# Performance work log

Hardware: AMD Instinct MI355X
Metric: run time of the kernel (lower is better)

Reference implementation:

```python
import jax, jax.numpy as jnp
import numpy as np

B, C, H, Wd = 4, 2048, 64, 64
HID = 256


def setup_inputs() -> dict:
    key = jax.random.key(0)
    k1, k2, k3, k4 = jax.random.split(key, 4)
    return {
        "query_features": jax.random.normal(k1, (B, C, H, Wd), dtype=jnp.float32),
        "prompt_features": jax.random.normal(k2, (B, C, H, Wd), dtype=jnp.float32),
        "W": jax.random.normal(k3, (HID, C), dtype=jnp.float32) * (1.0 / np.sqrt(C)),
        "b": jax.random.normal(k4, (HID,), dtype=jnp.float32) * 0.02,
    }


def reference(query_features, prompt_features, W, b):
    # 1x1 conv == channel projection
    Q = jnp.einsum('bchw,oc->bohw', query_features, W) + b[None, :, None, None]
    K = jnp.einsum('bchw,oc->bohw', prompt_features, W) + b[None, :, None, None]
    Bq, Cf, Hq, Wq = prompt_features.shape
    V = prompt_features.reshape(Bq, Cf, Hq * Wq)              # b c p
    # full pairwise score tensor: bijkl -> b i j (k l)
    attn = jnp.einsum('bcij,bckl->bijkl', Q, K).reshape(Bq, Hq, Wq, Hq * Wq)
    attn = jax.nn.softmax(attn, axis=3)
    aligned = jnp.einsum('bijp,bcp->bcij', attn, V)           # b c h w
    return aligned
```

## Files before the change

### kernel.cpp

```cpp
#include <hip/hip_runtime.h>
#include <math.h>


#define BATCH 4
#define CH    2048
#define PP    4096
#define DD    256

typedef __bf16    bf16x8 __attribute__((ext_vector_type(8)));
typedef _Float16  f16x8  __attribute__((ext_vector_type(8)));
typedef _Float16  f16x4  __attribute__((ext_vector_type(4)));
typedef float     f32x4  __attribute__((ext_vector_type(4)));

__device__ __forceinline__ unsigned short f2bf(float f) {
  unsigned int u = __float_as_uint(f);
  unsigned int r = u + 0x7fffu + ((u >> 16) & 1u);
  return (unsigned short)(r >> 16);
}

#define GLL(src, dst) \
  __builtin_amdgcn_global_load_lds( \
      (const __attribute__((address_space(1))) unsigned int*)(uintptr_t)(src), \
      (__attribute__((address_space(3))) unsigned int*)(uintptr_t)(dst), 16, 0, 0)

__global__ __launch_bounds__(256) void prep_w(
    const float* __restrict__ W, _Float16* __restrict__ Wf) {
  int i = blockIdx.x * 256 + threadIdx.x;
  float4 v = ((const float4*)W)[i];
  f16x4 h = {(_Float16)v.x, (_Float16)v.y, (_Float16)v.z, (_Float16)v.w};
  ((f16x4*)Wf)[i] = h;
}

__global__ __launch_bounds__(256) void projX(
    const float* __restrict__ Xq, const float* __restrict__ Xp,
    const _Float16* __restrict__ Wf, const float* __restrict__ bias,
    unsigned short* __restrict__ Qh, unsigned short* __restrict__ Ql,
    unsigned short* __restrict__ Kh, unsigned short* __restrict__ Kl,
    unsigned short* __restrict__ Vb8, int zbase, int single) {
  const int z = zbase + blockIdx.z;
  const int b = z >> 1;
  const int ob = single ? 0 : b;
  const float* __restrict__ X =
      ((z & 1) ? Xp : Xq) + (size_t)b * CH * PP;
  unsigned short* __restrict__ Yh =
      ((z & 1) ? Kh : Qh) + (size_t)ob * PP * DD;
  unsigned short* __restrict__ Yl =
      ((z & 1) ? Kl : Ql) + (size_t)ob * PP * DD;
  unsigned short* __restrict__ Vb = Vb8 + (size_t)ob * CH * PP;
  const int emitV = (z & 1);

  const int pBase = blockIdx.x * 64;
  const int tid  = threadIdx.x;
  const int wave = tid >> 6;
  const int lane = tid & 63;
  const int row16 = lane & 15, quad = lane >> 4;

  __shared__ __align__(16) char LdsP[32768 + 16384];
  char*  Ws  = LdsP;
  float* LsX = (float*)(LdsP + 32768);

  const int wRowIn  = lane >> 3;
  const int wChunk  = (((lane & 7) ^ (lane >> 3)) << 4);
  const int xRowIn  = lane >> 4;
  const int xColB   = (lane & 15) * 16;

  f32x4 acc[4][4];
#pragma unroll
  for (int i = 0; i < 4; ++i)
#pragma unroll
    for (int j = 0; j < 4; ++j) acc[i][j] = (f32x4){0.f, 0.f, 0.f, 0.f};

#pragma unroll 1
  for (int c0 = 0; c0 < CH; c0 += 64) {
#pragma unroll
    for (int q = 0; q < 8; ++q) {
      const int g = wave * 8 + q;
      const char* src = (const char*)Wf +
          (size_t)(g * 8 + wRowIn) * (CH * 2) + c0 * 2 + wChunk;
      GLL(src, Ws + g * 1024);
    }
#pragma unroll
    for (int q = 0; q < 4; ++q) {
      const int g = wave * 4 + q;
      const char* src = (const char*)X +
          ((size_t)(c0 + g * 4 + xRowIn) * PP + pBase) * 4 + xColB;
      GLL(src, (char*)LsX + g * 1024);
    }
    __syncthreads();

#pragma unroll
    for (int s = 0; s < 2; ++s) {
      f16x8 af[4], bf[4];
#pragma unroll
      for (int i = 0; i < 4; ++i) {
        f16x8 a;
#pragma unroll
        for (int e = 0; e < 8; ++e)
          a[e] = (_Float16)LsX[(s * 32 + quad * 8 + e) * 64 + i * 16 + row16];
        af[i] = a;
      }
#pragma unroll
      for (int j = 0; j < 4; ++j) {
        const int brow = wave * 64 + j * 16 + row16;
        bf[j] = *(const f16x8*)(Ws + brow * 128 +
                                (((s * 4 + quad) ^ (row16 & 7)) << 4));
      }
#pragma unroll
      for (int i = 0; i < 4; ++i)
#pragma unroll
        for (int j = 0; j < 4; ++j)
          acc[i][j] = __builtin_amdgcn_mfma_f32_16x16x32_f16(
              af[i], bf[j], acc[i][j], 0, 0, 0);
    }

    if (emitV) {
      const int cl = tid >> 2, ps = (tid & 3) * 16;
      const float* xr = &LsX[cl * 64 + ps];
      unsigned short tmp[16];
#pragma unroll
      for (int u = 0; u < 16; ++u) tmp[u] = f2bf(xr[u]);
      char* dst = (char*)Vb + ((size_t)(c0 + cl) * PP + pBase + ps) * 2;
      *(uint4*)dst        = *(const uint4*)tmp;
      *(uint4*)(dst + 16) = *(const uint4*)(tmp + 8);
    }
    __syncthreads();
  }

#pragma unroll
  for (int i = 0; i < 4; ++i)
#pragma unroll
    for (int j = 0; j < 4; ++j) {
      const int ocol = wave * 64 + j * 16 + row16;
      const float bv = bias[ocol];
#pragma unroll
      for (int r = 0; r < 4; ++r) {
        const int prow = pBase + i * 16 + quad * 4 + r;
        float y = acc[i][j][r] + bv;
        unsigned short h = f2bf(y);
        float hf = __uint_as_float((unsigned int)h << 16);
        unsigned short l = f2bf(y - hf);
        Yh[(size_t)prow * DD + ocol] = h;
        Yl[(size_t)prow * DD + ocol] = l;
      }
    }
}

__global__ __launch_bounds__(256) void softmax8(float* __restrict__ S_) {
  float* __restrict__ Sb = S_ + (size_t)blockIdx.y * PP * PP;
  unsigned short* __restrict__ Ab = (unsigned short*)Sb;
  const size_t p = blockIdx.x;
  float* row = Sb + p * PP;
  const int tid = threadIdx.x;
  float4 v[4];
#pragma unroll
  for (int i = 0; i < 4; ++i)
    v[i] = *(const float4*)&row[(i * 256 + tid) * 4];
  float m = -1e30f;
#pragma unroll
  for (int i = 0; i < 4; ++i)
    m = fmaxf(m, fmaxf(fmaxf(v[i].x, v[i].y), fmaxf(v[i].z, v[i].w)));
#pragma unroll
  for (int off = 32; off > 0; off >>= 1)
    m = fmaxf(m, __shfl_xor(m, off));
  __shared__ float red[4];
  const int lane = tid & 63, wv = tid >> 6;
  if (lane == 0) red[wv] = m;
  __syncthreads();
  m = fmaxf(fmaxf(red[0], red[1]), fmaxf(red[2], red[3]));
  __syncthreads();
  float s = 0.f;
#pragma unroll
  for (int i = 0; i < 4; ++i) {
    v[i].x = __expf(v[i].x - m);
    v[i].y = __expf(v[i].y - m);
    v[i].z = __expf(v[i].z - m);
    v[i].w = __expf(v[i].w - m);
    s += v[i].x + v[i].y + v[i].z + v[i].w;
  }
#pragma unroll
  for (int off = 32; off > 0; off >>= 1)
    s += __shfl_xor(s, off);
  if (lane == 0) red[wv] = s;
  __syncthreads();
  s = red[0] + red[1] + red[2] + red[3];
  const float inv = 1.f / s;
  unsigned short* orow = Ab + p * 8192;
#pragma unroll
  for (int i = 0; i < 4; ++i) {
    ushort4 o;
    o.x = f2bf(v[i].x * inv); o.y = f2bf(v[i].y * inv);
    o.z = f2bf(v[i].z * inv); o.w = f2bf(v[i].w * inv);
    *(ushort4*)&orow[(i * 256 + tid) * 4] = o;
  }
}


#define AOFF(d, h) ((d) * 32768 + (h) * 16384)
#define BOFF(d, h) (65536 + (d) * 32768 + (h) * 16384)

#define PH_READ_A(d, mh) do {                                                  \
  _Pragma("unroll")                                                            \
  for (int m_ = 0; m_ < 4; ++m_) {                                             \
    const int ro_ = AOFF(d, wm) + ((mh) * 64 + m_ * 16 + row16) * 128;         \
    aR[m_][0] = *(const bf16x8*)(Lds + ro_ + cx0);                             \
    aR[m_][1] = *(const bf16x8*)(Lds + ro_ + cx1);                             \
  } } while (0)

#define PH_READ_B(d, nh, breg) do {                                            \
  _Pragma("unroll")                                                            \
  for (int n_ = 0; n_ < 2; ++n_) {                                             \
    const int ro_ = BOFF(d, wnh) + (wnl * 64 + (nh) * 32 + n_ * 16 + row16) * 128; \
    breg[n_][0] = *(const bf16x8*)(Lds + ro_ + cx0);                           \
    breg[n_][1] = *(const bf16x8*)(Lds + ro_ + cx1);                           \
  } } while (0)

#define PH_MFMA(mh, nh, breg) do {                                             \
  __builtin_amdgcn_s_setprio(1);                                               \
  _Pragma("unroll")                                                            \
  for (int m_ = 0; m_ < 4; ++m_)                                               \
  _Pragma("unroll")                                                            \
  for (int n_ = 0; n_ < 2; ++n_) {                                             \
    f32x4 a_ = acc[(mh) * 4 + m_][(nh) * 2 + n_];                              \
    a_ = __builtin_amdgcn_mfma_f32_16x16x32_bf16(aR[m_][0], breg[n_][0], a_, 0, 0, 0); \
    a_ = __builtin_amdgcn_mfma_f32_16x16x32_bf16(aR[m_][1], breg[n_][1], a_, 0, 0, 0); \
    acc[(mh) * 4 + m_][(nh) * 2 + n_] = a_;                                    \
  }                                                                            \
  __builtin_amdgcn_s_setprio(0); } while (0)

#define PH_MFMA3(mh, nh, breg) do {                                            \
  __builtin_amdgcn_s_setprio(1);                                               \
  _Pragma("unroll")                                                            \
  for (int m_ = 0; m_ < 4; ++m_)                                               \
  _Pragma("unroll")                                                            \
  for (int n_ = 0; n_ < 2; ++n_) {                                             \
    f32x4 a_ = acc[(mh) * 4 + m_][(nh) * 2 + n_];                              \
    a_ = __builtin_amdgcn_mfma_f32_16x16x32_bf16(aR[m_][0], breg[n_][0], a_, 0, 0, 0); \
    a_ = __builtin_amdgcn_mfma_f32_16x16x32_bf16(aR[m_][0], breg[n_][1], a_, 0, 0, 0); \
    a_ = __builtin_amdgcn_mfma_f32_16x16x32_bf16(aR[m_][1], breg[n_][0], a_, 0, 0, 0); \
    acc[(mh) * 4 + m_][(nh) * 2 + n_] = a_;                                    \
  }                                                                            \
  __builtin_amdgcn_s_setprio(0); } while (0)

#define BAR_MID() do {                                                         \
  __builtin_amdgcn_sched_barrier(0);                                           \
  __builtin_amdgcn_s_barrier();                                                \
  asm volatile("s_waitcnt lgkmcnt(0)" ::: "memory");                           \
  __builtin_amdgcn_sched_barrier(0); } while (0)

#define BAR_END() __builtin_amdgcn_s_barrier()

__global__ __launch_bounds__(512, 2) void out8(
    const unsigned short* __restrict__ V_,
    const unsigned short* __restrict__ A_,
    float* __restrict__ O_) {
  const size_t z = blockIdx.z;
  const unsigned short* __restrict__ Vb = V_ + z * (size_t)CH * PP;
  const unsigned short* __restrict__ Ab = A_ + z * (size_t)PP * 8192;
  float* __restrict__ Ob = O_ + z * (size_t)CH * PP;

  const int pBase = blockIdx.x * 256;
  const int cBase = blockIdx.y * 256;
  const int tid = threadIdx.x;
  const int wave = tid >> 6, lane = tid & 63;
  const int wm = wave >> 2;
  const int wn = wave & 3;
  const int wnh = wn >> 1, wnl = wn & 1;
  const int row16 = lane & 15, quad = lane >> 4;

  __shared__ __align__(16) char Lds[131072];

  const int swz = (row16 & 7) << 4;
  const int cx0 = ((quad) << 4) ^ swz;
  const int cx1 = ((4 + quad) << 4) ^ swz;

  const int stRow0 = (wave * 2 + 0) * 8 + (lane >> 3);
  const int stRow1 = (wave * 2 + 1) * 8 + (lane >> 3);
  const int stCol  = (((lane & 7) ^ (lane >> 3)) << 4);
  char* ldsSt0 = Lds + (wave * 2 + 0) * 1024;
  char* ldsSt1 = Lds + (wave * 2 + 1) * 1024;

  const size_t VLDG = (size_t)PP * 2;
  const size_t ALDG = (size_t)8192 * 2;

  auto STG = [&](int ldsOff, const void* gbase, size_t ldgB, int rowBase, int gkB) {
    const char* g0 = (const char*)gbase + (size_t)(rowBase + stRow0) * ldgB + gkB + stCol;
    const char* g1 = (const char*)gbase + (size_t)(rowBase + stRow1) * ldgB + gkB + stCol;
    GLL(g0, ldsSt0 + ldsOff);
    GLL(g1, ldsSt1 + ldsOff);
  };

  f32x4 acc[8][4];
#pragma unroll
  for (int i = 0; i < 8; ++i)
#pragma unroll
    for (int j = 0; j < 4; ++j) acc[i][j] = (f32x4){0.f, 0.f, 0.f, 0.f};

  bf16x8 aR[4][2], bLo[2][2], bHi[2][2];

  STG(BOFF(0, 0), Ab, ALDG, pBase + 0,   0);
  STG(BOFF(0, 1), Ab, ALDG, pBase + 128, 0);
  STG(AOFF(0, 0), Vb, VLDG, cBase + 0,   0);
  STG(AOFF(0, 1), Vb, VLDG, cBase + 128, 0);
  STG(BOFF(1, 0), Ab, ALDG, pBase + 0,   128);
  STG(BOFF(1, 1), Ab, ALDG, pBase + 128, 128);
  asm volatile("s_waitcnt vmcnt(4)" ::: "memory");
  __builtin_amdgcn_s_barrier();

#pragma unroll 1
  for (int i = 0; i < 31; ++i) {
    const int t = 2 * i;
    const int gk1 = (t + 1) * 128, gk2 = (t + 2) * 128, gk3 = (t + 3) * 128;
    PH_READ_A(0, 0); PH_READ_B(0, 0, bLo);
    STG(AOFF(1, 0), Vb, VLDG, cBase + 0, gk1);
    BAR_MID(); PH_MFMA(0, 0, bLo); BAR_END();
    PH_READ_B(0, 1, bHi);
    STG(AOFF(1, 1), Vb, VLDG, cBase + 128, gk1);
    BAR_MID(); PH_MFMA(0, 1, bHi); BAR_END();
    PH_READ_A(0, 1);
    STG(BOFF(0, 0), Ab, ALDG, pBase + 0, gk2);
    BAR_MID(); PH_MFMA(1, 0, bLo); BAR_END();
    STG(BOFF(0, 1), Ab, ALDG, pBase + 128, gk2);
    BAR_MID(); PH_MFMA(1, 1, bHi);
    asm volatile("s_waitcnt vmcnt(4)" ::: "memory");
    BAR_END();
    PH_READ_A(1, 0); PH_READ_B(1, 0, bLo);
    STG(AOFF(0, 0), Vb, VLDG, cBase + 0, gk2);
    BAR_MID(); PH_MFMA(0, 0, bLo); BAR_END();
    PH_READ_B(1, 1, bHi);
    STG(AOFF(0, 1), Vb, VLDG, cBase + 128, gk2);
    BAR_MID(); PH_MFMA(0, 1, bHi); BAR_END();
    PH_READ_A(1, 1);
    STG(BOFF(1, 0), Ab, ALDG, pBase + 0, gk3);
    BAR_MID(); PH_MFMA(1, 0, bLo); BAR_END();
    STG(BOFF(1, 1), Ab, ALDG, pBase + 128, gk3);
    BAR_MID(); PH_MFMA(1, 1, bHi);
    asm volatile("s_waitcnt vmcnt(4)" ::: "memory");
    BAR_END();
  }

  {
    const int gk1 = 63 * 128;
    PH_READ_A(0, 0); PH_READ_B(0, 0, bLo);
    STG(AOFF(1, 0), Vb, VLDG, cBase + 0, gk1);
    BAR_MID(); PH_MFMA(0, 0, bLo); BAR_END();
    PH_READ_B(0, 1, bHi);
    STG(AOFF(1, 1), Vb, VLDG, cBase + 128, gk1);
    BAR_MID(); PH_MFMA(0, 1, bHi); BAR_END();
    PH_READ_A(0, 1);
    BAR_MID(); PH_MFMA(1, 0, bLo); BAR_END();
    BAR_MID(); PH_MFMA(1, 1, bHi);
    asm volatile("s_waitcnt vmcnt(0)" ::: "memory");
    BAR_END();
    PH_READ_A(1, 0); PH_READ_B(1, 0, bLo);
    BAR_MID(); PH_MFMA(0, 0, bLo); BAR_END();
    PH_READ_B(1, 1, bHi);
    BAR_MID(); PH_MFMA(0, 1, bHi); BAR_END();
    PH_READ_A(1, 1);
    BAR_MID(); PH_MFMA(1, 0, bLo); BAR_END();
    BAR_MID(); PH_MFMA(1, 1, bHi);
  }

#pragma unroll
  for (int mi = 0; mi < 8; ++mi)
#pragma unroll
    for (int nj = 0; nj < 4; ++nj) {
      const int col = pBase + wn * 64 + nj * 16 + row16;
      float* orow = Ob + (size_t)(cBase + wm * 128 + mi * 16 + quad * 4) * PP + col;
#pragma unroll
      for (int r = 0; r < 4; ++r)
        orow[(size_t)r * PP] = acc[mi][nj][r];
    }
}

__global__ __launch_bounds__(512, 2) void scr8(
    const unsigned short* __restrict__ Qh_, const unsigned short* __restrict__ Ql_,
    const unsigned short* __restrict__ Kh_, const unsigned short* __restrict__ Kl_,
    float* __restrict__ S_) {
  const size_t z = blockIdx.z;
  const unsigned short* __restrict__ Qh = Qh_ + z * (size_t)PP * DD;
  const unsigned short* __restrict__ Ql = Ql_ + z * (size_t)PP * DD;
  const unsigned short* __restrict__ Kh = Kh_ + z * (size_t)PP * DD;
  const unsigned short* __restrict__ Kl = Kl_ + z * (size_t)PP * DD;
  float* __restrict__ S = S_ + z * (size_t)PP * PP;

  const int kBase = blockIdx.x * 256;
  const int pBase = blockIdx.y * 256;
  const int tid = threadIdx.x;
  const int wave = tid >> 6, lane = tid & 63;
  const int wm = wave >> 2;
  const int wn = wave & 3;
  const int wnh = wn >> 1, wnl = wn & 1;
  const int row16 = lane & 15, quad = lane >> 4;

  __shared__ __align__(16) char Lds[131072];

  const int swz = (row16 & 7) << 4;
  const int cx0 = ((quad) << 4) ^ swz;
  const int cx1 = ((4 + quad) << 4) ^ swz;

  const int stRow0 = (wave * 2 + 0) * 8 + (lane >> 3);
  const int stRow1 = (wave * 2 + 1) * 8 + (lane >> 3);
  const int cc   = (lane & 7) ^ (lane >> 3);
  const int ccB  = (cc & 3) * 16;
  const char* tQ = (const char*)((cc >> 2) ? Ql : Qh);
  const char* tK = (const char*)((cc >> 2) ? Kl : Kh);
  char* ldsSt0 = Lds + (wave * 2 + 0) * 1024;
  char* ldsSt1 = Lds + (wave * 2 + 1) * 1024;

  auto STG = [&](int ldsOff, const char* tbase, int rowBase, int tkB) {
    const char* g0 = tbase + (size_t)(rowBase + stRow0) * 512 + tkB + ccB;
    const char* g1 = tbase + (size_t)(rowBase + stRow1) * 512 + tkB + ccB;
    GLL(g0, ldsSt0 + ldsOff);
    GLL(g1, ldsSt1 + ldsOff);
  };

  f32x4 acc[8][4];
#pragma unroll
  for (int i = 0; i < 8; ++i)
#pragma unroll
    for (int j = 0; j < 4; ++j) acc[i][j] = (f32x4){0.f, 0.f, 0.f, 0.f};

  bf16x8 aR[4][2], bLo[2][2], bHi[2][2];

  STG(BOFF(0, 0), tK, kBase + 0,   0);
  STG(BOFF(0, 1), tK, kBase + 128, 0);
  STG(AOFF(0, 0), tQ, pBase + 0,   0);
  STG(AOFF(0, 1), tQ, pBase + 128, 0);
  STG(BOFF(1, 0), tK, kBase + 0,   64);
  STG(BOFF(1, 1), tK, kBase + 128, 64);
  asm volatile("s_waitcnt vmcnt(4)" ::: "memory");
  __builtin_amdgcn_s_barrier();

#pragma unroll 1
  for (int i = 0; i < 3; ++i) {
    const int t = 2 * i;
    const int gk1 = (t + 1) * 64, gk2 = (t + 2) * 64, gk3 = (t + 3) * 64;
    PH_READ_A(0, 0); PH_READ_B(0, 0, bLo);
    STG(AOFF(1, 0), tQ, pBase + 0, gk1);
    BAR_MID(); PH_MFMA3(0, 0, bLo); BAR_END();
    PH_READ_B(0, 1, bHi);
    STG(AOFF(1, 1), tQ, pBase + 128, gk1);
    BAR_MID(); PH_MFMA3(0, 1, bHi); BAR_END();
    PH_READ_A(0, 1);
    STG(BOFF(0, 0), tK, kBase + 0, gk2);
    BAR_MID(); PH_MFMA3(1, 0, bLo); BAR_END();
    STG(BOFF(0, 1), tK, kBase + 128, gk2);
    BAR_MID(); PH_MFMA3(1, 1, bHi);
    asm volatile("s_waitcnt vmcnt(4)" ::: "memory");
    BAR_END();
    PH_READ_A(1, 0); PH_READ_B(1, 0, bLo);
    STG(AOFF(0, 0), tQ, pBase + 0, gk2);
    BAR_MID(); PH_MFMA3(0, 0, bLo); BAR_END();
    PH_READ_B(1, 1, bHi);
    STG(AOFF(0, 1), tQ, pBase + 128, gk2);
    BAR_MID(); PH_MFMA3(0, 1, bHi); BAR_END();
    PH_READ_A(1, 1);
    STG(BOFF(1, 0), tK, kBase + 0, gk3);
    BAR_MID(); PH_MFMA3(1, 0, bLo); BAR_END();
    STG(BOFF(1, 1), tK, kBase + 128, gk3);
    BAR_MID(); PH_MFMA3(1, 1, bHi);
    asm volatile("s_waitcnt vmcnt(4)" ::: "memory");
    BAR_END();
  }

  {
    const int gk1 = 7 * 64;
    PH_READ_A(0, 0); PH_READ_B(0, 0, bLo);
    STG(AOFF(1, 0), tQ, pBase + 0, gk1);
    BAR_MID(); PH_MFMA3(0, 0, bLo); BAR_END();
    PH_READ_B(0, 1, bHi);
    STG(AOFF(1, 1), tQ, pBase + 128, gk1);
    BAR_MID(); PH_MFMA3(0, 1, bHi); BAR_END();
    PH_READ_A(0, 1);
    BAR_MID(); PH_MFMA3(1, 0, bLo); BAR_END();
    BAR_MID(); PH_MFMA3(1, 1, bHi);
    asm volatile("s_waitcnt vmcnt(0)" ::: "memory");
    BAR_END();
    PH_READ_A(1, 0); PH_READ_B(1, 0, bLo);
    BAR_MID(); PH_MFMA3(0, 0, bLo); BAR_END();
    PH_READ_B(1, 1, bHi);
    BAR_MID(); PH_MFMA3(0, 1, bHi); BAR_END();
    PH_READ_A(1, 1);
    BAR_MID(); PH_MFMA3(1, 0, bLo); BAR_END();
    BAR_MID(); PH_MFMA3(1, 1, bHi);
  }

#pragma unroll
  for (int mi = 0; mi < 8; ++mi)
#pragma unroll
    for (int nj = 0; nj < 4; ++nj) {
      const int kcol = kBase + wn * 64 + nj * 16 + row16;
      float* orow = S + (size_t)(pBase + wm * 128 + mi * 16 + quad * 4) * PP + kcol;
#pragma unroll
      for (int r = 0; r < 4; ++r)
        orow[(size_t)r * PP] = acc[mi][nj][r];
    }
}

extern "C" void kernel_launch(void* const* d_in, const int* in_sizes, int n_in,
                              void* d_out, int out_size, void* d_ws, size_t ws_size,
                              hipStream_t stream) {
  const float* Xq   = (const float*)d_in[0];
  const float* Xp   = (const float*)d_in[1];
  const float* Wg   = (const float*)d_in[2];
  const float* bias = (const float*)d_in[3];
  float* out = (float*)d_out;

  char* w = (char*)d_ws;
  const size_t MB = 1024 * 1024;
  const size_t CHPP = (size_t)CH * PP;

  if (ws_size >= 354 * MB) {
    _Float16* Wf       = (_Float16*)w;
    unsigned short* Qh = (unsigned short*)(w + 1 * MB);
    unsigned short* Ql = (unsigned short*)(w + 9 * MB);
    unsigned short* Kh = (unsigned short*)(w + 17 * MB);
    unsigned short* Kl = (unsigned short*)(w + 25 * MB);
    unsigned short* Vbf = (unsigned short*)(w + 33 * MB);
    float* S           = (float*)(w + 97 * MB);

    prep_w<<<512, 256, 0, stream>>>(Wg, Wf);
    projX<<<dim3(PP / 64, 1, 2 * BATCH), 256, 0, stream>>>(
        Xq, Xp, Wf, bias, Qh, Ql, Kh, Kl, Vbf, 0, 0);
    scr8<<<dim3(PP / 256, PP / 256, BATCH), 512, 0, stream>>>(Qh, Ql, Kh, Kl, S);
    softmax8<<<dim3(PP, BATCH), 256, 0, stream>>>(S);
    out8<<<dim3(PP / 256, CH / 256, BATCH), 512, 0, stream>>>(
        Vbf, (unsigned short*)S, out);
  } else {
    _Float16* Wf       = (_Float16*)w;
    unsigned short* Qh = (unsigned short*)(w + 1 * MB);
    unsigned short* Ql = (unsigned short*)(w + 3 * MB);
    unsigned short* Kh = (unsigned short*)(w + 5 * MB);
    unsigned short* Kl = (unsigned short*)(w + 7 * MB);
    unsigned short* Vbf = (unsigned short*)(w + 9 * MB);
    float* S           = (float*)(w + 25 * MB);

    prep_w<<<512, 256, 0, stream>>>(Wg, Wf);
    for (int b = 0; b < BATCH; ++b) {
      projX<<<dim3(PP / 64, 1, 2), 256, 0, stream>>>(
          Xq, Xp, Wf, bias, Qh, Ql, Kh, Kl, Vbf, 2 * b, 1);
      scr8<<<dim3(PP / 256, PP / 256, 1), 512, 0, stream>>>(Qh, Ql, Kh, Kl, S);
      softmax8<<<dim3(PP, 1), 256, 0, stream>>>(S);
      out8<<<dim3(PP / 256, CH / 256, 1), 512, 0, stream>>>(
          Vbf, (unsigned short*)S, out + (size_t)b * CHPP);
    }
  }
}
```

Before: 730.8 us.

## Prefetch X into registers and stage fp16 transposed tile in LDS for projection

The projection kernel now loads the next 64-channel slice of X into registers while the current slice is being used. It converts the values to fp16 on the fly and writes them to LDS in a transposed, padded layout, so the MFMA A-fragments become single 16-byte LDS reads instead of eight scalar float reads with per-element conversion. The V bf16 emission now comes straight from registers, and hand-placed waitcnt and barriers overlap global loads with compute. The risks are extra register pressure from the double-buffered float4s and fragile manual vmcnt counts, which could go wrong if the compiler reorders memory operations.

```diff
diff --git a/kernel.cpp b/kernel.cpp
--- a/kernel.cpp
+++ b/kernel.cpp
@@ -16,6 +16,13 @@
   unsigned int u = __float_as_uint(f);
   unsigned int r = u + 0x7fffu + ((u >> 16) & 1u);
   return (unsigned short)(r >> 16);
+}
+
+__device__ __forceinline__ unsigned int h16(float f) {
+  _Float16 h = (_Float16)f;
+  unsigned short u;
+  __builtin_memcpy(&u, &h, 2);
+  return (unsigned int)u;
 }
 
 #define GLL(src, dst) \
@@ -31,7 +38,7 @@
   ((f16x4*)Wf)[i] = h;
 }
 
-__global__ __launch_bounds__(256) void projX(
+__global__ __launch_bounds__(256) void projXk(
     const float* __restrict__ Xq, const float* __restrict__ Xp,
     const _Float16* __restrict__ Wf, const float* __restrict__ bias,
     unsigned short* __restrict__ Qh, unsigned short* __restrict__ Ql,
@@ -54,15 +61,15 @@
   const int wave = tid >> 6;
   const int lane = tid & 63;
   const int row16 = lane & 15, quad = lane >> 4;
-
-  __shared__ __align__(16) char LdsP[32768 + 16384];
-  char*  Ws  = LdsP;
-  float* LsX = (float*)(LdsP + 32768);
+  const int iL = tid & 15;
+  const int vL = tid >> 4;
+
+  __shared__ __align__(16) char LdsP[32768 + 9216];
+  char* Ws = LdsP;
+  unsigned int* LsT = (unsigned int*)(LdsP + 32768);
 
   const int wRowIn  = lane >> 3;
   const int wChunk  = (((lane & 7) ^ (lane >> 3)) << 4);
-  const int xRowIn  = lane >> 4;
-  const int xColB   = (lane & 15) * 16;
 
   f32x4 acc[4][4];
 #pragma unroll
@@ -70,35 +77,60 @@
 #pragma unroll
     for (int j = 0; j < 4; ++j) acc[i][j] = (f32x4){0.f, 0.f, 0.f, 0.f};
 
+  const float* Xl = X + (size_t)(4 * vL) * PP + pBase + 4 * iL;
+
+  float4 xv[4], xn[4];
+#pragma unroll
+  for (int cc = 0; cc < 4; ++cc)
+    xv[cc] = *(const float4*)(Xl + (size_t)cc * PP);
+  __builtin_amdgcn_sched_barrier(0);
+
 #pragma unroll 1
-  for (int c0 = 0; c0 < CH; c0 += 64) {
+  for (int c0 = 0; c0 < CH - 64; c0 += 64) {
 #pragma unroll
     for (int q = 0; q < 8; ++q) {
       const int g = wave * 8 + q;
-      const char* src = (const char*)Wf +
-          (size_t)(g * 8 + wRowIn) * (CH * 2) + c0 * 2 + wChunk;
-      GLL(src, Ws + g * 1024);
-    }
-#pragma unroll
-    for (int q = 0; q < 4; ++q) {
-      const int g = wave * 4 + q;
-      const char* src = (const char*)X +
-          ((size_t)(c0 + g * 4 + xRowIn) * PP + pBase) * 4 + xColB;
-      GLL(src, (char*)LsX + g * 1024);
-    }
-    __syncthreads();
-
+      GLL((const char*)Wf + (size_t)(g * 8 + wRowIn) * (CH * 2) + c0 * 2 + wChunk,
+          Ws + g * 1024);
+    }
+    __builtin_amdgcn_sched_barrier(0);
+#pragma unroll
+    for (int cc = 0; cc < 4; ++cc)
+      xn[cc] = *(const float4*)(Xl + (size_t)(c0 + 64 + cc) * PP);
+    __builtin_amdgcn_sched_barrier(0);
+#pragma unroll
+    for (int r = 0; r < 4; ++r) {
+      const float a0 = ((const float*)&xv[0])[r];
+      const float a1 = ((const float*)&xv[1])[r];
+      const float a2 = ((const float*)&xv[2])[r];
+      const float a3 = ((const float*)&xv[3])[r];
+      unsigned long long w = (unsigned long long)(h16(a0) | (h16(a1) << 16)) |
+                             ((unsigned long long)(h16(a2) | (h16(a3) << 16)) << 32);
+      *(unsigned long long*)&LsT[(4 * iL + r) * 36 + 2 * vL] = w;
+    }
+    if (emitV) {
+#pragma unroll
+      for (int cc = 0; cc < 4; ++cc) {
+        float4 v = xv[cc];
+        ushort4 o = {f2bf(v.x), f2bf(v.y), f2bf(v.z), f2bf(v.w)};
+        *(ushort4*)&Vb[(size_t)(c0 + 4 * vL + cc) * PP + pBase + 4 * iL] = o;
+      }
+    }
+    __builtin_amdgcn_sched_barrier(0);
+    if (emitV) {
+      asm volatile("s_waitcnt vmcnt(8) lgkmcnt(0)" ::: "memory");
+    } else {
+      asm volatile("s_waitcnt vmcnt(4) lgkmcnt(0)" ::: "memory");
+    }
+    __builtin_amdgcn_s_barrier();
+    __builtin_amdgcn_sched_barrier(0);
 #pragma unroll
     for (int s = 0; s < 2; ++s) {
       f16x8 af[4], bf[4];
 #pragma unroll
-      for (int i = 0; i < 4; ++i) {
-        f16x8 a;
-#pragma unroll
-        for (int e = 0; e < 8; ++e)
-          a[e] = (_Float16)LsX[(s * 32 + quad * 8 + e) * 64 + i * 16 + row16];
-        af[i] = a;
-      }
+      for (int i = 0; i < 4; ++i)
+        af[i] = *(const f16x8*)((const char*)LsT +
+                                (i * 16 + row16) * 144 + s * 64 + quad * 16);
 #pragma unroll
       for (int j = 0; j < 4; ++j) {
         const int brow = wave * 64 + j * 16 + row16;
@@ -112,18 +144,67 @@
           acc[i][j] = __builtin_amdgcn_mfma_f32_16x16x32_f16(
               af[i], bf[j], acc[i][j], 0, 0, 0);
     }
-
+    __builtin_amdgcn_sched_barrier(0);
+    __builtin_amdgcn_s_barrier();
+#pragma unroll
+    for (int cc = 0; cc < 4; ++cc) xv[cc] = xn[cc];
+  }
+
+  {
+    const int c0 = CH - 64;
+#pragma unroll
+    for (int q = 0; q < 8; ++q) {
+      const int g = wave * 8 + q;
+      GLL((const char*)Wf + (size_t)(g * 8 + wRowIn) * (CH * 2) + c0 * 2 + wChunk,
+          Ws + g * 1024);
+    }
+    __builtin_amdgcn_sched_barrier(0);
+#pragma unroll
+    for (int r = 0; r < 4; ++r) {
+      const float a0 = ((const float*)&xv[0])[r];
+      const float a1 = ((const float*)&xv[1])[r];
+      const float a2 = ((const float*)&xv[2])[r];
+      const float a3 = ((const float*)&xv[3])[r];
+      unsigned long long w = (unsigned long long)(h16(a0) | (h16(a1) << 16)) |
+                             ((unsigned long long)(h16(a2) | (h16(a3) << 16)) << 32);
+      *(unsigned long long*)&LsT[(4 * iL + r) * 36 + 2 * vL] = w;
+    }
     if (emitV) {
-      const int cl = tid >> 2, ps = (tid & 3) * 16;
-      const float* xr = &LsX[cl * 64 + ps];
-      unsigned short tmp[16];
-#pragma unroll
-      for (int u = 0; u < 16; ++u) tmp[u] = f2bf(xr[u]);
-      char* dst = (char*)Vb + ((size_t)(c0 + cl) * PP + pBase + ps) * 2;
-      *(uint4*)dst        = *(const uint4*)tmp;
-      *(uint4*)(dst + 16) = *(const uint4*)(tmp + 8);
-    }
-    __syncthreads();
+#pragma unroll
+      for (int cc = 0; cc < 4; ++cc) {
+        float4 v = xv[cc];
+        ushort4 o = {f2bf(v.x), f2bf(v.y), f2bf(v.z), f2bf(v.w)};
+        *(ushort4*)&Vb[(size_t)(c0 + 4 * vL + cc) * PP + pBase + 4 * iL] = o;
+      }
+    }
+    __builtin_amdgcn_sched_barrier(0);
+    if (emitV) {
+      asm volatile("s_waitcnt vmcnt(4) lgkmcnt(0)" ::: "memory");
+    } else {
+      asm volatile("s_waitcnt vmcnt(0) lgkmcnt(0)" ::: "memory");
+    }
+    __builtin_amdgcn_s_barrier();
+    __builtin_amdgcn_sched_barrier(0);
+#pragma unroll
+    for (int s = 0; s < 2; ++s) {
+      f16x8 af[4], bf[4];
+#pragma unroll
+      for (int i = 0; i < 4; ++i)
+        af[i] = *(const f16x8*)((const char*)LsT +
+                                (i * 16 + row16) * 144 + s * 64 + quad * 16);
+#pragma unroll
+      for (int j = 0; j < 4; ++j) {
+        const int brow = wave * 64 + j * 16 + row16;
+        bf[j] = *(const f16x8*)(Ws + brow * 128 +
+                                (((s * 4 + quad) ^ (row16 & 7)) << 4));
+      }
+#pragma unroll
+      for (int i = 0; i < 4; ++i)
+#pragma unroll
+        for (int j = 0; j < 4; ++j)
+          acc[i][j] = __builtin_amdgcn_mfma_f32_16x16x32_f16(
+              af[i], bf[j], acc[i][j], 0, 0, 0);
+    }
   }
 
 #pragma unroll
@@ -520,7 +601,7 @@
     float* S           = (float*)(w + 97 * MB);
 
     prep_w<<<512, 256, 0, stream>>>(Wg, Wf);
-    projX<<<dim3(PP / 64, 1, 2 * BATCH), 256, 0, stream>>>(
+    projXk<<<dim3(PP / 64, 1, 2 * BATCH), 256, 0, stream>>>(
         Xq, Xp, Wf, bias, Qh, Ql, Kh, Kl, Vbf, 0, 0);
     scr8<<<dim3(PP / 256, PP / 256, BATCH), 512, 0, stream>>>(Qh, Ql, Kh, Kl, S);
     softmax8<<<dim3(PP, BATCH), 256, 0, stream>>>(S);
@@ -537,7 +618,7 @@
 
     prep_w<<<512, 256, 0, stream>>>(Wg, Wf);
     for (int b = 0; b < BATCH; ++b) {
-      projX<<<dim3(PP / 64, 1, 2), 256, 0, stream>>>(
+      projXk<<<dim3(PP / 64, 1, 2), 256, 0, stream>>>(
           Xq, Xp, Wf, bias, Qh, Ql, Kh, Kl, Vbf, 2 * b, 1);
       scr8<<<dim3(PP / 256, PP / 256, 1), 512, 0, stream>>>(Qh, Ql, Kh, Kl, S);
       softmax8<<<dim3(PP, 1), 256, 0, stream>>>(S);
```

Result: no change. 735.2 us (+0.6%).
